# Performance work log

Hardware: AMD Instinct MI355X
Metric: run time of the kernel (lower is better)

## Reference

```python
import jax, jax.numpy as jnp
import numpy as np

N, K, D = 524288, 32, 64


def setup_inputs() -> dict:
    key = jax.random.key(0)
    k1, k2 = jax.random.split(key)
    X = jax.random.normal(k1, (N, D), dtype=jnp.float32)
    mu = jax.random.uniform(k2, (K, D), dtype=jnp.float32)
    var = jnp.ones((K, D), dtype=jnp.float32)
    pi = jnp.ones((K, 1), dtype=jnp.float32) / K  # uniform mixture weights, as in __init__
    return {"X": X, "mu": mu, "var": var, "pi": pi}


def reference(X, mu, var, pi):
    # One EM iteration (the body of GaussianMixture.fit).
    n = X.shape[0]
    log2pi = jnp.log(jnp.asarray(2.0 * np.pi, dtype=X.dtype))
    inv_var = 1.0 / var  # (K, D)
    # log_pk[k, n] = sum_d log N(x_nd; mu_kd, var_kd), via quadratic expansion
    # (same math as the broadcast (K, N, D) tensor, without materializing it).
    quad = (
        jnp.einsum("kd,nd->kn", inv_var, X * X)
        - 2.0 * jnp.einsum("kd,nd->kn", mu * inv_var, X)
        + jnp.sum(mu * mu * inv_var, axis=-1, keepdims=True)
    )  # (K, N)
    log_det = jnp.sum(jnp.log(var) + log2pi, axis=-1, keepdims=True)  # (K, 1)
    log_pk = -0.5 * (quad + log_det)  # (K, N)
    # E-step: responsibilities via stable logsumexp over components
    log_post = jnp.log(pi) + log_pk  # (K, N)
    log_norm = jax.scipy.special.logsumexp(log_post, axis=0, keepdims=True)
    r = jnp.exp(log_post - log_norm)  # (K, N)
    # M-step
    dem = jnp.sum(r, axis=1, keepdims=True)  # (K, 1)
    pi_new = dem / n
    rx = r @ X            # (K, D)
    rx2 = r @ (X * X)     # (K, D)
    mu_new = rx / dem
    # sum_n r_kn (x_nd - mu_new_kd)^2 = rx2 - 2 mu_new * rx + mu_new^2 * dem
    var_new = (rx2 - 2.0 * mu_new * rx + mu_new * mu_new * dem) / dem
    return jnp.concatenate([pi_new, mu_new, var_new], axis=1)  # (K, 1 + 2D)
```

## Files before the change

### kernel.cpp

```cpp
#include <hip/hip_runtime.h>
#include <hip/hip_bf16.h>
#include <math.h>
#include <string.h>

#define NPTS 524288
#define KC 32
#define DIM 64
#define NTILES 4096
#define PROW 4128
#define GRIDX 512

typedef __attribute__((ext_vector_type(8)))  short short8v;
typedef __attribute__((ext_vector_type(16))) float f32x16;

#define RL_BASE  32768
#define WL_BASE  40960
#define CL_BASE  49152
#define SMEM_BYTES 49280

__device__ __forceinline__ short f2bf(float f) {
    unsigned u = __float_as_uint(f);
    unsigned r = (u + 0x7FFFu + ((u >> 16) & 1u)) >> 16;
    return (short)r;
}
__device__ __forceinline__ unsigned short s2bf(float a) {
    __hip_bfloat16 h = __float2bfloat16(a);
    unsigned short u;
    memcpy(&u, &h, 2);
    return u;
}
__device__ __forceinline__ unsigned pk2bf(float a, float b) {
    return (unsigned)s2bf(a) | ((unsigned)s2bf(b) << 16);
}

__global__ void gmm_prep(const float* __restrict__ mu, const float* __restrict__ var,
                         const float* __restrict__ pi, short* __restrict__ W,
                         float* __restrict__ C) {
    int t = threadIdx.x + blockIdx.x * blockDim.x;
    if (t < KC * 128) {
        int k = t >> 7, d = t & 127;
        float iv = 1.0f / var[k * DIM + (d & 63)];
        float v = (d < DIM) ? mu[k * DIM + d] * iv : -0.5f * iv;
        W[t] = f2bf(v);
    }
    if (t < KC) {
        const float LOG2PI = 1.8378770664093453f;
        float s = 0.0f;
        for (int d = 0; d < DIM; ++d) {
            float v = var[t * DIM + d];
            float m = mu[t * DIM + d];
            s += m * m / v + logf(v);
        }
        C[t] = logf(pi[t]) - 0.5f * (s + DIM * LOG2PI);
    }
}

__device__ __forceinline__ void stage_chunk(unsigned char* smem, int w, int c, float4 v, int l) {
    int pt   = w * 32 + c * 4 + (l >> 4);
    int colB = (l & 15) * 8;
    int swz  = (pt & 15) << 4;
    uint2 bx, bx2;
    bx.x  = pk2bf(v.x, v.y);              bx.y  = pk2bf(v.z, v.w);
    bx2.x = pk2bf(v.x * v.x, v.y * v.y);  bx2.y = pk2bf(v.z * v.z, v.w * v.w);
    *(uint2*)(smem + pt * 256 + (colB ^ swz))         = bx;
    *(uint2*)(smem + pt * 256 + ((128 + colB) ^ swz)) = bx2;
}

__global__ __launch_bounds__(256, 2)
void gmm_main(const float* __restrict__ X, const short* __restrict__ W,
              const float* __restrict__ C, float* __restrict__ partials, int g) {
    __shared__ unsigned char smem[SMEM_BYTES];

    const int tid = threadIdx.x;
    const int l   = tid & 63;
    const int w   = tid >> 6;
    const int lm  = l & 31;
    const int lh  = l >> 5;

    {
        const uint4* W16 = (const uint4*)W;
#pragma unroll
        for (int i = 0; i < 2; ++i) {
            int idx  = tid * 2 + i;
            int row  = idx >> 4, slot = idx & 15;
            *(uint4*)(smem + WL_BASE + row * 256 + ((slot * 16) ^ ((row & 15) << 4))) = W16[idx];
        }
    }
    if (tid < KC) ((float*)(smem + CL_BASE))[tid] = C[tid];

    short8v onesf;
#pragma unroll
    for (int j = 0; j < 8; ++j) onesf[j] = (short)0x3F80;

    f32x16 rxacc, demA;
#pragma unroll
    for (int i = 0; i < 16; ++i) { rxacc[i] = 0.0f; demA[i] = 0.0f; }

    const float4* X4 = (const float4*)X;
    const int mypt = w * 32 + lm;

    float4 xr[8];
    {
        const float4* xs = X4 + (size_t)blockIdx.x * 2048 + w * 512;
#pragma unroll
        for (int c = 0; c < 8; ++c) xr[c] = xs[c * 64 + l];
    }

    __syncthreads();

    const float* cl = (const float*)(smem + CL_BASE);

    for (int tile = blockIdx.x; tile < NTILES; tile += g) {
#pragma unroll
        for (int c = 0; c < 8; ++c) stage_chunk(smem, w, c, xr[c], l);

        f32x16 s;
#pragma unroll
        for (int r = 0; r < 16; ++r) s[r] = 0.0f;
#pragma unroll
        for (int ks = 0; ks < 8; ++ks) {
            short8v a = *(const short8v*)(smem + WL_BASE + lm * 256 +
                                          ((ks * 32 + lh * 16) ^ ((lm & 15) << 4)));
            short8v b = *(const short8v*)(smem + mypt * 256 +
                                          ((ks * 32 + lh * 16) ^ ((lm & 15) << 4)));
            s = __builtin_amdgcn_mfma_f32_32x32x16_bf16(a, b, s, 0, 0, 0);
        }

#pragma unroll
        for (int r = 0; r < 16; ++r) s[r] += cl[(r & 3) + 8 * (r >> 2) + 4 * lh];
        float m = s[0];
#pragma unroll
        for (int r = 1; r < 16; ++r) m = fmaxf(m, s[r]);
        m = fmaxf(m, __shfl_xor(m, 32, 64));
        float sum = 0.0f;
#pragma unroll
        for (int r = 0; r < 16; ++r) { s[r] = __expf(s[r] - m); sum += s[r]; }
        sum += __shfl_xor(sum, 32, 64);
        float inv = 1.0f / sum;
#pragma unroll
        for (int r = 0; r < 16; ++r) {
            float rv = s[r] * inv;
            int comp = (r & 3) + 8 * (r >> 2) + 4 * lh;
            *(unsigned short*)(smem + RL_BASE + comp * 256 +
                               ((mypt * 2) ^ ((comp & 15) << 4))) = s2bf(rv);
        }
        __syncthreads();

        if (tile + g < NTILES) {
            const float4* xs = X4 + (size_t)(tile + g) * 2048 + w * 512;
#pragma unroll
            for (int c = 0; c < 8; ++c) xr[c] = xs[c * 64 + l];
        }

#pragma unroll
        for (int ks = 0; ks < 8; ++ks) {
            short8v af = *(const short8v*)(smem + RL_BASE + lm * 256 +
                                           ((ks * 32 + lh * 16) ^ ((lm & 15) << 4)));
            short8v bv;
#pragma unroll
            for (int j = 0; j < 8; ++j) {
                int pt = ks * 16 + lh * 8 + j;
                bv[j] = *(const short*)(smem + pt * 256 +
                                        ((mypt * 2) ^ ((pt & 15) << 4)));
            }
            rxacc = __builtin_amdgcn_mfma_f32_32x32x16_bf16(af, bv, rxacc, 0, 0, 0);
            demA  = __builtin_amdgcn_mfma_f32_32x32x16_bf16(af, onesf, demA, 0, 0, 0);
        }
        __syncthreads();
    }

    float* P = partials + (size_t)blockIdx.x * PROW;
#pragma unroll
    for (int r = 0; r < 16; ++r) {
        int comp = (r & 3) + 8 * (r >> 2) + 4 * lh;
        P[32 + comp * 128 + w * 32 + lm] = rxacc[r];
    }
    if (w == 0 && lm == 0) {
#pragma unroll
        for (int r = 0; r < 16; ++r)
            P[(r & 3) + 8 * (r >> 2) + 4 * lh] = demA[r];
    }
}

__global__ __launch_bounds__(512)
void gmm_reduce(const float* __restrict__ partials, float* __restrict__ out, int nb) {
    __shared__ float red[512 * 4];
    __shared__ float dred[512];
    __shared__ float rxf[128];
    const int k = blockIdx.x;
    const int t = threadIdx.x;
    const int f4i   = t & 31;
    const int chunk = t >> 5;

    float4 s4 = {0.f, 0.f, 0.f, 0.f};
    const int R = nb >> 4;
#pragma unroll 4
    for (int j = 0; j < R; ++j) {
        int b = chunk * R + j;
        float4 v = *((const float4*)(partials + (size_t)b * PROW + 32 + k * 128) + f4i);
        s4.x += v.x; s4.y += v.y; s4.z += v.z; s4.w += v.w;
    }
    float dp = 0.0f;
    for (int b = t; b < nb; b += 512) dp += partials[(size_t)b * PROW + k];

    *(float4*)(red + t * 4) = s4;
    dred[t] = dp;
    __syncthreads();
    for (int off = 256; off >= 1; off >>= 1) {
        if (t < off) dred[t] += dred[t + off];
        __syncthreads();
    }
    if (t < 32) {
        float4 a = {0.f, 0.f, 0.f, 0.f};
#pragma unroll
        for (int c = 0; c < 16; ++c) {
            float4 v = *(const float4*)(red + (c * 32 + t) * 4);
            a.x += v.x; a.y += v.y; a.z += v.z; a.w += v.w;
        }
        *(float4*)(rxf + t * 4) = a;
    }
    __syncthreads();
    float dem = dred[0];
    if (t < 64) {
        float inv = 1.0f / dem;
        float rx  = rxf[t];
        float rx2 = rxf[t + 64];
        float mu  = rx * inv;
        float va  = rx2 * inv - mu * mu;
        out[k * 129 + 1 + t]  = mu;
        out[k * 129 + 65 + t] = va;
        if (t == 0) out[k * 129] = dem * (1.0f / (float)NPTS);
    }
}

extern "C" void kernel_launch(void* const* d_in, const int* in_sizes, int n_in,
                              void* d_out, int out_size, void* d_ws, size_t ws_size,
                              hipStream_t stream) {
    const float* X   = (const float*)d_in[0];
    const float* mu  = (const float*)d_in[1];
    const float* var = (const float*)d_in[2];
    const float* pi  = (const float*)d_in[3];

    short* W        = (short*)d_ws;
    float* C        = (float*)((char*)d_ws + 8192);
    float* partials = (float*)((char*)d_ws + 8320);
    float* out      = (float*)d_out;

    int g = GRIDX;
    while (g > 64 && (size_t)8320 + (size_t)g * PROW * 4 > ws_size) g >>= 1;

    gmm_prep<<<16, 256, 0, stream>>>(mu, var, pi, W, C);
    gmm_main<<<g, 256, 0, stream>>>(X, W, C, partials, g);
    gmm_reduce<<<KC, 512, 0, stream>>>(partials, out, g);
}
```

Measured before the change: 45.10 us.

## Fuse prep into main kernel, hold weights in registers, double-buffer LDS tiles

```diff
diff --git a/kernel.cpp b/kernel.cpp
--- a/kernel.cpp
+++ b/kernel.cpp
@@ -13,10 +13,9 @@
 typedef __attribute__((ext_vector_type(8)))  short short8v;
 typedef __attribute__((ext_vector_type(16))) float f32x16;
 
-#define RL_BASE  32768
-#define WL_BASE  40960
-#define CL_BASE  49152
-#define SMEM_BYTES 49280
+#define BUFSZ 40960
+#define RLOFF 32768
+#define SMEM_BYTES 81920
 
 __device__ __forceinline__ short f2bf(float f) {
     unsigned u = __float_as_uint(f);
@@ -33,42 +32,21 @@
     return (unsigned)s2bf(a) | ((unsigned)s2bf(b) << 16);
 }
 
-__global__ void gmm_prep(const float* __restrict__ mu, const float* __restrict__ var,
-                         const float* __restrict__ pi, short* __restrict__ W,
-                         float* __restrict__ C) {
-    int t = threadIdx.x + blockIdx.x * blockDim.x;
-    if (t < KC * 128) {
-        int k = t >> 7, d = t & 127;
-        float iv = 1.0f / var[k * DIM + (d & 63)];
-        float v = (d < DIM) ? mu[k * DIM + d] * iv : -0.5f * iv;
-        W[t] = f2bf(v);
-    }
-    if (t < KC) {
-        const float LOG2PI = 1.8378770664093453f;
-        float s = 0.0f;
-        for (int d = 0; d < DIM; ++d) {
-            float v = var[t * DIM + d];
-            float m = mu[t * DIM + d];
-            s += m * m / v + logf(v);
-        }
-        C[t] = logf(pi[t]) - 0.5f * (s + DIM * LOG2PI);
-    }
-}
-
-__device__ __forceinline__ void stage_chunk(unsigned char* smem, int w, int c, float4 v, int l) {
+__device__ __forceinline__ void stage_chunk(unsigned char* xt, int w, int c, float4 v, int l) {
     int pt   = w * 32 + c * 4 + (l >> 4);
     int colB = (l & 15) * 8;
     int swz  = (pt & 15) << 4;
     uint2 bx, bx2;
     bx.x  = pk2bf(v.x, v.y);              bx.y  = pk2bf(v.z, v.w);
     bx2.x = pk2bf(v.x * v.x, v.y * v.y);  bx2.y = pk2bf(v.z * v.z, v.w * v.w);
-    *(uint2*)(smem + pt * 256 + (colB ^ swz))         = bx;
-    *(uint2*)(smem + pt * 256 + ((128 + colB) ^ swz)) = bx2;
+    *(uint2*)(xt + pt * 256 + (colB ^ swz))         = bx;
+    *(uint2*)(xt + pt * 256 + ((128 + colB) ^ swz)) = bx2;
 }
 
 __global__ __launch_bounds__(256, 2)
-void gmm_main(const float* __restrict__ X, const short* __restrict__ W,
-              const float* __restrict__ C, float* __restrict__ partials, int g) {
+void gmm_main(const float* __restrict__ X, const float* __restrict__ mu,
+              const float* __restrict__ var, const float* __restrict__ pi,
+              float* __restrict__ partials, int g) {
     __shared__ unsigned char smem[SMEM_BYTES];
 
     const int tid = threadIdx.x;
@@ -76,28 +54,10 @@
     const int w   = tid >> 6;
     const int lm  = l & 31;
     const int lh  = l >> 5;
-
-    {
-        const uint4* W16 = (const uint4*)W;
-#pragma unroll
-        for (int i = 0; i < 2; ++i) {
-            int idx  = tid * 2 + i;
-            int row  = idx >> 4, slot = idx & 15;
-            *(uint4*)(smem + WL_BASE + row * 256 + ((slot * 16) ^ ((row & 15) << 4))) = W16[idx];
-        }
-    }
-    if (tid < KC) ((float*)(smem + CL_BASE))[tid] = C[tid];
-
-    short8v onesf;
-#pragma unroll
-    for (int j = 0; j < 8; ++j) onesf[j] = (short)0x3F80;
-
-    f32x16 rxacc, demA;
-#pragma unroll
-    for (int i = 0; i < 16; ++i) { rxacc[i] = 0.0f; demA[i] = 0.0f; }
+    const int mypt = w * 32 + lm;
 
     const float4* X4 = (const float4*)X;
-    const int mypt = w * 32 + lm;
+    const int nt = NTILES / g;
 
     float4 xr[8];
     {
@@ -106,68 +66,118 @@
         for (int c = 0; c < 8; ++c) xr[c] = xs[c * 64 + l];
     }
 
-    __syncthreads();
-
-    const float* cl = (const float*)(smem + CL_BASE);
-
-    for (int tile = blockIdx.x; tile < NTILES; tile += g) {
-#pragma unroll
-        for (int c = 0; c < 8; ++c) stage_chunk(smem, w, c, xr[c], l);
-
-        f32x16 s;
-#pragma unroll
-        for (int r = 0; r < 16; ++r) s[r] = 0.0f;
-#pragma unroll
-        for (int ks = 0; ks < 8; ++ks) {
-            short8v a = *(const short8v*)(smem + WL_BASE + lm * 256 +
-                                          ((ks * 32 + lh * 16) ^ ((lm & 15) << 4)));
-            short8v b = *(const short8v*)(smem + mypt * 256 +
-                                          ((ks * 32 + lh * 16) ^ ((lm & 15) << 4)));
-            s = __builtin_amdgcn_mfma_f32_32x32x16_bf16(a, b, s, 0, 0, 0);
+    float* clp = (float*)(smem + BUFSZ + RLOFF);
+    float* cl  = (float*)(smem + BUFSZ + RLOFF + 1024);
+    {
+        int comp = tid >> 3, i8 = tid & 7;
+        const float* vv = var + comp * DIM + i8 * 8;
+        const float* mm = mu  + comp * DIM + i8 * 8;
+        float p = 0.0f;
+#pragma unroll
+        for (int j = 0; j < 8; ++j) { float v = vv[j], m2 = mm[j]; p += m2 * m2 / v + logf(v); }
+        clp[tid] = p;
+    }
+    __syncthreads();
+    if (tid < KC) {
+        float ssum = 0.0f;
+#pragma unroll
+        for (int j = 0; j < 8; ++j) ssum += clp[tid * 8 + j];
+        const float LOG2PI = 1.8378770664093453f;
+        cl[tid] = logf(pi[tid]) - 0.5f * (ssum + DIM * LOG2PI);
+    }
+    __syncthreads();
+    float cvec[16];
+#pragma unroll
+    for (int r = 0; r < 16; ++r) cvec[r] = cl[(r & 3) + 8 * (r >> 2) + 4 * lh];
+
+    short8v wf[8];
+#pragma unroll
+    for (int ks = 0; ks < 8; ++ks) {
+        int d0 = (ks & 3) * 16 + lh * 8;
+        float4 va = *(const float4*)(var + lm * DIM + d0);
+        float4 vb = *(const float4*)(var + lm * DIM + d0 + 4);
+        float vv[8] = { va.x, va.y, va.z, va.w, vb.x, vb.y, vb.z, vb.w };
+        if (ks < 4) {
+            float4 ma = *(const float4*)(mu + lm * DIM + d0);
+            float4 mb = *(const float4*)(mu + lm * DIM + d0 + 4);
+            float mm[8] = { ma.x, ma.y, ma.z, ma.w, mb.x, mb.y, mb.z, mb.w };
+#pragma unroll
+            for (int j = 0; j < 8; ++j) wf[ks][j] = f2bf(mm[j] / vv[j]);
+        } else {
+#pragma unroll
+            for (int j = 0; j < 8; ++j) wf[ks][j] = f2bf(-0.5f / vv[j]);
         }
-
-#pragma unroll
-        for (int r = 0; r < 16; ++r) s[r] += cl[(r & 3) + 8 * (r >> 2) + 4 * lh];
-        float m = s[0];
-#pragma unroll
-        for (int r = 1; r < 16; ++r) m = fmaxf(m, s[r]);
-        m = fmaxf(m, __shfl_xor(m, 32, 64));
-        float sum = 0.0f;
-#pragma unroll
-        for (int r = 0; r < 16; ++r) { s[r] = __expf(s[r] - m); sum += s[r]; }
-        sum += __shfl_xor(sum, 32, 64);
-        float inv = 1.0f / sum;
-#pragma unroll
-        for (int r = 0; r < 16; ++r) {
-            float rv = s[r] * inv;
-            int comp = (r & 3) + 8 * (r >> 2) + 4 * lh;
-            *(unsigned short*)(smem + RL_BASE + comp * 256 +
-                               ((mypt * 2) ^ ((comp & 15) << 4))) = s2bf(rv);
-        }
-        __syncthreads();
-
-        if (tile + g < NTILES) {
-            const float4* xs = X4 + (size_t)(tile + g) * 2048 + w * 512;
-#pragma unroll
-            for (int c = 0; c < 8; ++c) xr[c] = xs[c * 64 + l];
-        }
-
-#pragma unroll
-        for (int ks = 0; ks < 8; ++ks) {
-            short8v af = *(const short8v*)(smem + RL_BASE + lm * 256 +
-                                           ((ks * 32 + lh * 16) ^ ((lm & 15) << 4)));
-            short8v bv;
-#pragma unroll
-            for (int j = 0; j < 8; ++j) {
-                int pt = ks * 16 + lh * 8 + j;
-                bv[j] = *(const short*)(smem + pt * 256 +
-                                        ((mypt * 2) ^ ((pt & 15) << 4)));
-            }
-            rxacc = __builtin_amdgcn_mfma_f32_32x32x16_bf16(af, bv, rxacc, 0, 0, 0);
-            demA  = __builtin_amdgcn_mfma_f32_32x32x16_bf16(af, onesf, demA, 0, 0, 0);
-        }
-        __syncthreads();
-    }
+    }
+
+    short8v onesf;
+#pragma unroll
+    for (int j = 0; j < 8; ++j) onesf[j] = (short)0x3F80;
+
+    f32x16 rxacc, demA;
+#pragma unroll
+    for (int i = 0; i < 16; ++i) { rxacc[i] = 0.0f; demA[i] = 0.0f; }
+
+#define TILE_BODY(b, j)                                                              \
+    {                                                                                \
+        unsigned char* xt = smem + (b) * BUFSZ;                                      \
+        unsigned char* rl = smem + (b) * BUFSZ + RLOFF;                              \
+        _Pragma("unroll")                                                            \
+        for (int c = 0; c < 8; ++c) stage_chunk(xt, w, c, xr[c], l);                 \
+        f32x16 s;                                                                    \
+        _Pragma("unroll")                                                            \
+        for (int r = 0; r < 16; ++r) s[r] = 0.0f;                                    \
+        _Pragma("unroll")                                                            \
+        for (int ks = 0; ks < 8; ++ks) {                                             \
+            short8v bfr = *(const short8v*)(xt + mypt * 256 +                        \
+                            ((ks * 32 + lh * 16) ^ ((lm & 15) << 4)));               \
+            s = __builtin_amdgcn_mfma_f32_32x32x16_bf16(wf[ks], bfr, s, 0, 0, 0);    \
+        }                                                                            \
+        _Pragma("unroll")                                                            \
+        for (int r = 0; r < 16; ++r) s[r] += cvec[r];                                \
+        float mx = s[0];                                                             \
+        _Pragma("unroll")                                                            \
+        for (int r = 1; r < 16; ++r) mx = fmaxf(mx, s[r]);                           \
+        mx = fmaxf(mx, __shfl_xor(mx, 32, 64));                                      \
+        float sum = 0.0f;                                                            \
+        _Pragma("unroll")                                                            \
+        for (int r = 0; r < 16; ++r) { s[r] = __expf(s[r] - mx); sum += s[r]; }      \
+        sum += __shfl_xor(sum, 32, 64);                                              \
+        float inv = 1.0f / sum;                                                      \
+        _Pragma("unroll")                                                            \
+        for (int r = 0; r < 16; ++r) {                                               \
+            float rv = s[r] * inv;                                                   \
+            int comp = (r & 3) + 8 * (r >> 2) + 4 * lh;                              \
+            *(unsigned short*)(rl + comp * 256 +                                     \
+                ((mypt * 2) ^ ((comp & 15) << 4))) = s2bf(rv);                       \
+        }                                                                            \
+        __syncthreads();                                                             \
+        if ((j) + 1 < nt) {                                                          \
+            const float4* xs = X4 +                                                  \
+                (size_t)(blockIdx.x + ((j) + 1) * g) * 2048 + w * 512;               \
+            _Pragma("unroll")                                                        \
+            for (int c = 0; c < 8; ++c) xr[c] = xs[c * 64 + l];                      \
+        }                                                                            \
+        _Pragma("unroll")                                                            \
+        for (int ks = 0; ks < 8; ++ks) {                                             \
+            short8v af = *(const short8v*)(rl + lm * 256 +                           \
+                            ((ks * 32 + lh * 16) ^ ((lm & 15) << 4)));               \
+            short8v bv;                                                              \
+            _Pragma("unroll")                                                        \
+            for (int jj = 0; jj < 8; ++jj) {                                         \
+                int pt = ks * 16 + lh * 8 + jj;                                      \
+                bv[jj] = *(const short*)(xt + pt * 256 +                             \
+                            ((mypt * 2) ^ ((pt & 15) << 4)));                        \
+            }                                                                        \
+            rxacc = __builtin_amdgcn_mfma_f32_32x32x16_bf16(af, bv, rxacc, 0, 0, 0); \
+            demA  = __builtin_amdgcn_mfma_f32_32x32x16_bf16(af, onesf, demA, 0, 0, 0);\
+        }                                                                            \
+    }
+
+    for (int j = 0; j < nt; j += 2) {
+        TILE_BODY(0, j);
+        TILE_BODY(1, j + 1);
+    }
+#undef TILE_BODY
 
     float* P = partials + (size_t)blockIdx.x * PROW;
 #pragma unroll
@@ -225,9 +235,9 @@
         float inv = 1.0f / dem;
         float rx  = rxf[t];
         float rx2 = rxf[t + 64];
-        float mu  = rx * inv;
-        float va  = rx2 * inv - mu * mu;
-        out[k * 129 + 1 + t]  = mu;
+        float muv = rx * inv;
+        float va  = rx2 * inv - muv * muv;
+        out[k * 129 + 1 + t]  = muv;
         out[k * 129 + 65 + t] = va;
         if (t == 0) out[k * 129] = dem * (1.0f / (float)NPTS);
     }
@@ -241,15 +251,12 @@
     const float* var = (const float*)d_in[2];
     const float* pi  = (const float*)d_in[3];
 
-    short* W        = (short*)d_ws;
-    float* C        = (float*)((char*)d_ws + 8192);
-    float* partials = (float*)((char*)d_ws + 8320);
+    float* partials = (float*)d_ws;
     float* out      = (float*)d_out;
 
     int g = GRIDX;
-    while (g > 64 && (size_t)8320 + (size_t)g * PROW * 4 > ws_size) g >>= 1;
-
-    gmm_prep<<<16, 256, 0, stream>>>(mu, var, pi, W, C);
-    gmm_main<<<g, 256, 0, stream>>>(X, W, C, partials, g);
+    while (g > 64 && (size_t)g * PROW * 4 > ws_size) g >>= 1;
+
+    gmm_main<<<g, 256, 0, stream>>>(X, mu, var, pi, partials, g);
     gmm_reduce<<<KC, 512, 0, stream>>>(partials, out, g);
 }
```

Result: slower. 97.41 us (+116.0%).
